# Kernel tuning notes

Hardware: AMD Instinct MI355X
Metric: run time of the kernel (lower is better)

## Reference

```python
import jax, jax.numpy as jnp
import numpy as np

C = 256
C8 = C // 8

def setup_inputs() -> dict:
    key = jax.random.key(0)
    ks = jax.random.split(key, 8)
    a = jax.random.normal(ks[0], (4, C, 64, 64), dtype=jnp.float32)
    s = 1.0 / np.sqrt(C)
    b_w = jax.random.normal(ks[1], (C8, C), dtype=jnp.float32) * s
    b_b = jnp.zeros((C8,), dtype=jnp.float32)
    c_w = jax.random.normal(ks[2], (C8, C), dtype=jnp.float32) * s
    c_b = jnp.zeros((C8,), dtype=jnp.float32)
    d_w = jax.random.normal(ks[3], (C, C), dtype=jnp.float32) * s
    d_b = jnp.zeros((C,), dtype=jnp.float32)
    alpha = jnp.zeros((1,), dtype=jnp.float32) + 0.5  # nonzero so attention path is exercised
    return {"a": a, "b_w": b_w, "b_b": b_b, "c_w": c_w, "c_b": c_b, "d_w": d_w, "d_b": d_b, "alpha": alpha}

def _conv1x1(x, w, b):
    # x: [n, c, h, w], w: [o, c] -> [n, o, h, w]
    return jnp.einsum('nchw,oc->nohw', x, w) + b[None, :, None, None]

def reference(a, b_w, b_b, c_w, c_b, d_w, d_b, alpha):
    n, chan, h, w = a.shape
    nhw = h * w
    b = _conv1x1(a, b_w, b_b).reshape(n, -1, nhw)   # [n, C/8, nhw]
    c = _conv1x1(a, c_w, c_b).reshape(n, -1, nhw)   # [n, C/8, nhw]
    k = jnp.einsum('nci,ncj->nij', b, c)            # [n, nhw, nhw]
    s = jax.nn.softmax(k, axis=-1)
    d = _conv1x1(a, d_w, d_b).reshape(n, -1, nhw)   # [n, C, nhw]
    kl = jnp.einsum('ncj,nij->nci', d, s)           # d @ s^T
    kl = kl.reshape(n, chan, h, w)
    return alpha * kl + a
```

## Files before the change

### kernel.cpp

```cpp
#include <hip/hip_runtime.h>
#include <hip/hip_bf16.h>

#define CCH 256
#define CQK 32
#define NHW 4096

typedef float f32x4 __attribute__((ext_vector_type(4)));
typedef _Float16 hv8 __attribute__((ext_vector_type(8)));
typedef _Float16 hv4 __attribute__((ext_vector_type(4)));
typedef __fp16 fv2 __attribute__((ext_vector_type(2)));

typedef __attribute__((address_space(3))) unsigned int lds_u32_t;
typedef __attribute__((address_space(1))) const unsigned int glb_u32_t;
__device__ __forceinline__ void gll16(const _Float16* gp, _Float16* lp) {
    __builtin_amdgcn_global_load_lds((glb_u32_t*)gp, (lds_u32_t*)lp, 16, 0, 0);
}

__global__ __launch_bounds__(256) void prep_kernel(
    const float* __restrict__ b_w, const float* __restrict__ c_w,
    const float* __restrict__ d_w, _Float16* __restrict__ Wh)
{
    const int bid = blockIdx.x, tid = threadIdx.x;
    const int idx = (bid * 256 + tid) * 4;
    const int row = idx >> 8, col = idx & 255;
    const float* src = (row < 32) ? (b_w + row * CCH + col)
                     : (row < 64) ? (c_w + (row - 32) * CCH + col)
                                  : (d_w + (row - 64) * CCH + col);
    const float scl = (row < 32) ? 1.4426950408889634f : 1.0f;
    float4 v = *reinterpret_cast<const float4*>(src);
    _Float16* dst = Wh + (size_t)row * CCH + col;
    dst[0] = (_Float16)(v.x * scl); dst[1] = (_Float16)(v.y * scl);
    dst[2] = (_Float16)(v.z * scl); dst[3] = (_Float16)(v.w * scl);
}

__global__ __launch_bounds__(256) void proj_kernel(
    const float* __restrict__ a, const _Float16* __restrict__ Wh,
    const float* __restrict__ b_b, const float* __restrict__ c_b,
    const float* __restrict__ d_b,
    _Float16* __restrict__ bqT, _Float16* __restrict__ ckT,
    _Float16* __restrict__ dv)
{
    __shared__ _Float16 aT[32][CCH + 24];

    const int n    = blockIdx.x >> 7;
    const int i0   = (blockIdx.x & 127) << 5;
    const int tid  = threadIdx.x;
    const int lane = tid & 63;
    const int wave = tid >> 6;
    const int l15  = lane & 15;
    const int quad = lane >> 4;

    {
        const float* ap = a + (size_t)(n*CCH + tid)*NHW + i0;
        #pragma unroll
        for (int j = 0; j < 8; ++j) {
            float4 v = *reinterpret_cast<const float4*>(ap + j*4);
            aT[j*4+0][tid] = (_Float16)v.x;
            aT[j*4+1][tid] = (_Float16)v.y;
            aT[j*4+2][tid] = (_Float16)v.z;
            aT[j*4+3][tid] = (_Float16)v.w;
        }
    }
    __syncthreads();

    const f32x4 zf = {0.f, 0.f, 0.f, 0.f};
    f32x4 acc[5][2];
    #pragma unroll
    for (int t = 0; t < 5; ++t) { acc[t][0] = zf; acc[t][1] = zf; }

    const int ch0w = wave * 80;

    #pragma unroll
    for (int ks = 0; ks < 8; ++ks) {
        const int k0 = ks * 32;
        hv8 af0 = *reinterpret_cast<const hv8*>(&aT[l15][k0 + quad*8]);
        hv8 af1 = *reinterpret_cast<const hv8*>(&aT[16 + l15][k0 + quad*8]);
        #pragma unroll
        for (int t = 0; t < 5; ++t) {
            const int ch0 = ch0w + t*16;
            hv8 bf = *reinterpret_cast<const hv8*>(
                Wh + (size_t)(ch0 + l15)*CCH + k0 + quad*8);
            acc[t][0] = __builtin_amdgcn_mfma_f32_16x16x32_f16(af0, bf, acc[t][0], 0, 0, 0);
            acc[t][1] = __builtin_amdgcn_mfma_f32_16x16x32_f16(af1, bf, acc[t][1], 0, 0, 0);
        }
    }

    const int pos_b = i0 + quad*4;
    #pragma unroll
    for (int t = 0; t < 5; ++t) {
        const int ch0 = ch0w + t*16;
        if (ch0 < 64) {
            const float* bias_arr = (ch0 < 32) ? b_b : c_b;
            _Float16*    outp     = (ch0 < 32) ? bqT : ckT;
            const int    ch       = (ch0 & 31) + l15;
            const float  bias     = bias_arr[ch] *
                ((ch0 < 32) ? 1.4426950408889634f : 1.0f);
            #pragma unroll
            for (int nf = 0; nf < 2; ++nf) {
                #pragma unroll
                for (int r = 0; r < 4; ++r) {
                    const int pos = pos_b + nf*16 + r;
                    outp[((size_t)n*NHW + pos)*CQK + ch] =
                        (_Float16)(acc[t][nf][r] + bias);
                }
            }
        } else {
            const int ch   = ch0 - 64 + l15;
            const float bias = d_b[ch];
            #pragma unroll
            for (int nf = 0; nf < 2; ++nf) {
                hv4 v = { (_Float16)(acc[t][nf][0] + bias),
                          (_Float16)(acc[t][nf][1] + bias),
                          (_Float16)(acc[t][nf][2] + bias),
                          (_Float16)(acc[t][nf][3] + bias) };
                *reinterpret_cast<hv4*>(
                    dv + ((size_t)n*CCH + ch)*NHW + pos_b + nf*16) = v;
            }
        }
    }
}

__global__ __launch_bounds__(512, 2) void attn_kernel(
    const _Float16* __restrict__ bqT, const _Float16* __restrict__ ckT,
    const _Float16* __restrict__ dv,
    const float* __restrict__ a, const float* __restrict__ alpha_p,
    float* __restrict__ out)
{
    __shared__ __align__(16) char smem[143360];

    const int bx   = ((blockIdx.x & 7) << 5) | (blockIdx.x >> 3);
    const int n    = bx >> 6;
    const int cg   = (bx >> 5) & 1;
    const int qt   = bx & 31;
    const int q0b  = qt << 7;
    const int co0  = cg << 7;
    const int tid  = threadIdx.x;
    const int wave = tid >> 6;
    const int g    = wave >> 1;
    const int qw   = wave & 1;
    const int lane = tid & 63;
    const int l15  = lane & 15;
    const int quad = lane >> 4;
    const int kg0  = g << 10;

    _Float16* vbuf = (_Float16*)(smem + (g << 14));
    _Float16* pb   = (_Float16*)(smem + 65536 + wave*9216);
    float*    lbuf = (float*)(smem + 139264);
    float*    mbuf = (float*)(smem + 141312);

    const f32x4 zf = {0.f, 0.f, 0.f, 0.f};
    const _Float16 one_h = (_Float16)1.0f;
    const hv8 ones = { one_h, one_h, one_h, one_h, one_h, one_h, one_h, one_h };

    hv8 qf[4];
    #pragma unroll
    for (int X = 0; X < 4; ++X) {
        const int q = q0b + qw*64 + X*16 + l15;
        qf[X] = *reinterpret_cast<const hv8*>(
            bqT + ((size_t)n*NHW + q)*CQK + quad*8);
    }

    const _Float16* ckbase = ckT + ((size_t)(n*NHW + kg0 + l15))*CQK + quad*8;

    float mneg[4] = {0.f, 0.f, 0.f, 0.f};

    f32x4 acc[4][8];
    #pragma unroll
    for (int X = 0; X < 4; ++X)
        #pragma unroll
        for (int t = 0; t < 8; ++t) acc[X][t] = zf;
    f32x4 accL[4];
    #pragma unroll
    for (int X = 0; X < 4; ++X) accL[X] = zf;

    const int rl8 = lane >> 3;
    const _Float16* dvs = dv
        + (size_t)(n*CCH + co0 + qw*64 + rl8)*NHW + kg0 + 8*((lane & 7) ^ rl8);
    _Float16* ldsb = (_Float16*)(smem + (g << 14) + qw*8192);

    const int c0h = ((quad*16) ^ ((l15 & 7) << 4)) >> 1;
    const int c1h = ((64 + quad*16) ^ ((l15 & 7) << 4)) >> 1;

    auto softmax_tile = [&](const hv8* kf) {
        #pragma unroll
        for (int X = 0; X < 4; ++X) {
            const f32x4 minit = {mneg[X], mneg[X], mneg[X], mneg[X]};
            f32x4 s0 = __builtin_amdgcn_mfma_f32_16x16x32_f16(kf[0], qf[X], minit, 0, 0, 0);
            f32x4 s1 = __builtin_amdgcn_mfma_f32_16x16x32_f16(kf[1], qf[X], minit, 0, 0, 0);
            f32x4 s2 = __builtin_amdgcn_mfma_f32_16x16x32_f16(kf[2], qf[X], minit, 0, 0, 0);
            f32x4 s3 = __builtin_amdgcn_mfma_f32_16x16x32_f16(kf[3], qf[X], minit, 0, 0, 0);
            float tm = fmaxf(
                fmaxf(fmaxf(fmaxf(s0[0], s0[1]), fmaxf(s0[2], s0[3])),
                      fmaxf(fmaxf(s1[0], s1[1]), fmaxf(s1[2], s1[3]))),
                fmaxf(fmaxf(fmaxf(s2[0], s2[1]), fmaxf(s2[2], s2[3])),
                      fmaxf(fmaxf(s3[0], s3[1]), fmaxf(s3[2], s3[3]))));
            tm = fmaxf(tm, __shfl_xor(tm, 16, 64));
            tm = fmaxf(tm, __shfl_xor(tm, 32, 64));
            const float upd = (tm > 8.0f) ? tm : 0.0f;
            if (__any(upd > 0.0f)) {
                const float sc = __builtin_amdgcn_exp2f(-upd);
                float s_r0 = __shfl(sc, quad*4 + 0, 64);
                float s_r1 = __shfl(sc, quad*4 + 1, 64);
                float s_r2 = __shfl(sc, quad*4 + 2, 64);
                float s_r3 = __shfl(sc, quad*4 + 3, 64);
                #pragma unroll
                for (int t = 0; t < 8; ++t) {
                    acc[X][t][0] *= s_r0; acc[X][t][1] *= s_r1;
                    acc[X][t][2] *= s_r2; acc[X][t][3] *= s_r3;
                }
                accL[X][0] *= s_r0; accL[X][1] *= s_r1;
                accL[X][2] *= s_r2; accL[X][3] *= s_r3;
                mneg[X] -= upd;
                s0[0] -= upd; s0[1] -= upd; s0[2] -= upd; s0[3] -= upd;
                s1[0] -= upd; s1[1] -= upd; s1[2] -= upd; s1[3] -= upd;
                s2[0] -= upd; s2[1] -= upd; s2[2] -= upd; s2[3] -= upd;
                s3[0] -= upd; s3[1] -= upd; s3[2] -= upd; s3[3] -= upd;
            }
            const f32x4 sv[4] = {s0, s1, s2, s3};
            #pragma unroll
            for (int f = 0; f < 4; ++f) {
                float p0 = __builtin_amdgcn_exp2f(sv[f][0]);
                float p1 = __builtin_amdgcn_exp2f(sv[f][1]);
                float p2 = __builtin_amdgcn_exp2f(sv[f][2]);
                float p3 = __builtin_amdgcn_exp2f(sv[f][3]);
                fv2 lo = __builtin_amdgcn_cvt_pkrtz(p0, p1);
                fv2 hi = __builtin_amdgcn_cvt_pkrtz(p2, p3);
                uint2 w;
                w.x = __builtin_bit_cast(unsigned, lo);
                w.y = __builtin_bit_cast(unsigned, hi);
                *reinterpret_cast<uint2*>(
                    pb + X*1152 + l15*72 + f*16 + quad*4) = w;
            }
        }
    };

    hv8 pf0[4], pf1[4];
    auto read_pf = [&]() {
        #pragma unroll
        for (int X = 0; X < 4; ++X) {
            pf0[X] = *reinterpret_cast<const hv8*>(pb + X*1152 + l15*72 + quad*8);
            pf1[X] = *reinterpret_cast<const hv8*>(pb + X*1152 + l15*72 + 32 + quad*8);
        }
    };

    auto stage = [&](int kt) {
        #pragma unroll
        for (int j = 0; j < 8; ++j)
            gll16(dvs + (size_t)(j*8)*NHW + kt*64, ldsb + (size_t)(j*8)*64);
    };

    auto load_kf = [&](int key0, hv8* kf) {
        #pragma unroll
        for (int f = 0; f < 4; ++f)
            kf[f] = *reinterpret_cast<const hv8*>(
                ckbase + (size_t)(key0 + f*16)*CQK);
    };

    {
        stage(0);
        hv8 kf0[4];
        load_kf(0, kf0);
        softmax_tile(kf0);
        read_pf();
    }
    __syncthreads();

    for (int kt = 0; kt < 16; ++kt) {
        hv8 kfn[4];
        if (kt < 15) load_kf((kt + 1)*64, kfn);

        #pragma unroll
        for (int t = 0; t < 8; ++t) {
            const _Float16* vr = vbuf + (t*16 + l15)*64;
            hv8 d0 = *reinterpret_cast<const hv8*>(vr + c0h);
            #pragma unroll
            for (int X = 0; X < 4; ++X)
                acc[X][t] = __builtin_amdgcn_mfma_f32_16x16x32_f16(
                    pf0[X], d0, acc[X][t], 0, 0, 0);
            hv8 d1 = *reinterpret_cast<const hv8*>(vr + c1h);
            #pragma unroll
            for (int X = 0; X < 4; ++X)
                acc[X][t] = __builtin_amdgcn_mfma_f32_16x16x32_f16(
                    pf1[X], d1, acc[X][t], 0, 0, 0);
        }
        #pragma unroll
        for (int X = 0; X < 4; ++X) {
            accL[X] = __builtin_amdgcn_mfma_f32_16x16x32_f16(pf0[X], ones, accL[X], 0, 0, 0);
            accL[X] = __builtin_amdgcn_mfma_f32_16x16x32_f16(pf1[X], ones, accL[X], 0, 0, 0);
        }

        if (kt < 15) {
            softmax_tile(kfn);
            __syncthreads();
            stage(kt + 1);
            read_pf();
            __syncthreads();
        }
    }

    if (lane < 16) {
        #pragma unroll
        for (int X = 0; X < 4; ++X)
            mbuf[g*128 + qw*64 + X*16 + l15] = -mneg[X];
    }
    __syncthreads();

    {
        #pragma unroll
        for (int X = 0; X < 4; ++X) {
            const int qloc = qw*64 + X*16 + quad*4;
            float4 m0 = *reinterpret_cast<float4*>(&mbuf[0*128 + qloc]);
            float4 m1 = *reinterpret_cast<float4*>(&mbuf[1*128 + qloc]);
            float4 m2 = *reinterpret_cast<float4*>(&mbuf[2*128 + qloc]);
            float4 m3 = *reinterpret_cast<float4*>(&mbuf[3*128 + qloc]);
            float4 mm;
            mm.x = fmaxf(fmaxf(m0.x, m1.x), fmaxf(m2.x, m3.x));
            mm.y = fmaxf(fmaxf(m0.y, m1.y), fmaxf(m2.y, m3.y));
            mm.z = fmaxf(fmaxf(m0.z, m1.z), fmaxf(m2.z, m3.z));
            mm.w = fmaxf(fmaxf(m0.w, m1.w), fmaxf(m2.w, m3.w));
            float4 mo = (g == 0) ? m0 : (g == 1) ? m1 : (g == 2) ? m2 : m3;
            float sc0 = __builtin_amdgcn_exp2f(mo.x - mm.x);
            float sc1 = __builtin_amdgcn_exp2f(mo.y - mm.y);
            float sc2 = __builtin_amdgcn_exp2f(mo.z - mm.z);
            float sc3 = __builtin_amdgcn_exp2f(mo.w - mm.w);
            #pragma unroll
            for (int t = 0; t < 8; ++t) {
                acc[X][t][0] *= sc0; acc[X][t][1] *= sc1;
                acc[X][t][2] *= sc2; acc[X][t][3] *= sc3;
            }
            accL[X][0] *= sc0; accL[X][1] *= sc1;
            accL[X][2] *= sc2; accL[X][3] *= sc3;
        }
    }

    float* buf1 = (float*)smem;
    float* buf2 = (float*)(smem + 67584);
    const int qloc = qw*64 + quad*4;

    if (l15 == 0) {
        #pragma unroll
        for (int X = 0; X < 4; ++X)
            *reinterpret_cast<float4*>(&lbuf[g*128 + qw*64 + X*16 + quad*4]) =
                *reinterpret_cast<float4*>(&accL[X]);
    }
    if (g == 1 || g == 3) {
        float* b = (g == 1) ? buf1 : buf2;
        #pragma unroll
        for (int X = 0; X < 4; ++X)
            #pragma unroll
            for (int t = 0; t < 8; ++t)
                *reinterpret_cast<float4*>(
                    &b[(t*16 + l15)*132 + qw*64 + X*16 + quad*4]) =
                    *reinterpret_cast<float4*>(&acc[X][t]);
    }
    __syncthreads();
    if (g == 0 || g == 2) {
        float* b = (g == 0) ? buf1 : buf2;
        #pragma unroll
        for (int X = 0; X < 4; ++X)
            #pragma unroll
            for (int t = 0; t < 8; ++t) {
                float4 p = *reinterpret_cast<float4*>(
                    &b[(t*16 + l15)*132 + qw*64 + X*16 + quad*4]);
                acc[X][t][0] += p.x; acc[X][t][1] += p.y;
                acc[X][t][2] += p.z; acc[X][t][3] += p.w;
            }
    }
    __syncthreads();
    if (g == 2) {
        #pragma unroll
        for (int X = 0; X < 4; ++X)
            #pragma unroll
            for (int t = 0; t < 8; ++t)
                *reinterpret_cast<float4*>(
                    &buf1[(t*16 + l15)*132 + qw*64 + X*16 + quad*4]) =
                    *reinterpret_cast<float4*>(&acc[X][t]);
    }
    __syncthreads();
    if (g == 0) {
        const float alpha = alpha_p[0];
        #pragma unroll
        for (int X = 0; X < 4; ++X) {
            const int qlocX = qw*64 + X*16 + quad*4;
            #pragma unroll
            for (int t = 0; t < 8; ++t) {
                float4 p = *reinterpret_cast<float4*>(
                    &buf1[(t*16 + l15)*132 + qlocX]);
                acc[X][t][0] += p.x; acc[X][t][1] += p.y;
                acc[X][t][2] += p.z; acc[X][t][3] += p.w;
            }
            float4 l0 = *reinterpret_cast<float4*>(&lbuf[0*128 + qlocX]);
            float4 l1 = *reinterpret_cast<float4*>(&lbuf[1*128 + qlocX]);
            float4 l2 = *reinterpret_cast<float4*>(&lbuf[2*128 + qlocX]);
            float4 l3 = *reinterpret_cast<float4*>(&lbuf[3*128 + qlocX]);
            f32x4 rl;
            rl[0] = alpha / (l0.x + l1.x + l2.x + l3.x);
            rl[1] = alpha / (l0.y + l1.y + l2.y + l3.y);
            rl[2] = alpha / (l0.z + l1.z + l2.z + l3.z);
            rl[3] = alpha / (l0.w + l1.w + l2.w + l3.w);
            #pragma unroll
            for (int t = 0; t < 8; ++t) {
                const size_t off =
                    ((size_t)(n*CCH + co0 + t*16 + l15))*NHW + q0b + qlocX;
                float4 av = *reinterpret_cast<const float4*>(a + off);
                float4 o;
                o.x = acc[X][t][0]*rl[0] + av.x;
                o.y = acc[X][t][1]*rl[1] + av.y;
                o.z = acc[X][t][2]*rl[2] + av.z;
                o.w = acc[X][t][3]*rl[3] + av.w;
                *reinterpret_cast<float4*>(out + off) = o;
            }
        }
    }
}

extern "C" void kernel_launch(void* const* d_in, const int* in_sizes, int n_in,
                              void* d_out, int out_size, void* d_ws, size_t ws_size,
                              hipStream_t stream)
{
    const float* a    = (const float*)d_in[0];
    const float* b_w  = (const float*)d_in[1];
    const float* b_b  = (const float*)d_in[2];
    const float* c_w  = (const float*)d_in[3];
    const float* c_b  = (const float*)d_in[4];
    const float* d_w  = (const float*)d_in[5];
    const float* d_b  = (const float*)d_in[6];
    const float* alp  = (const float*)d_in[7];
    float* out = (float*)d_out;

    _Float16* bqT  = (_Float16*)d_ws;
    _Float16* ckT  = bqT + (size_t)4*NHW*CQK;
    _Float16* dv   = ckT + (size_t)4*NHW*CQK;
    _Float16* Wh   = dv + (size_t)4*CCH*NHW;

    prep_kernel<<<80, 256, 0, stream>>>(b_w, c_w, d_w, Wh);
    proj_kernel<<<512, 256, 0, stream>>>(a, Wh, b_b, c_b, d_b, bqT, ckT, dv);
    attn_kernel<<<256, 512, 0, stream>>>(bqT, ckT, dv, a, alp, out);
}
```

Before: 165.0 us.

## Halve key tile to 32 and double-buffer V staging with one barrier per step

The key tile per iteration shrinks from 64 to 32 keys, so each step runs half the QK and PV MFMAs. The V tile staging becomes double-buffered: the next tile's global-to-LDS load is issued at the top of the iteration and overlaps the current compute. This removes one of the two __syncthreads per step, and the per-wave P buffer shrinks. The trade-off is twice as many iterations, more frequent softmax max checks and barriers, and shorter runs of MFMA work per sync.

After: 174.5 us. +5.8%, slower.

```diff
diff --git a/kernel.cpp b/kernel.cpp
--- a/kernel.cpp
+++ b/kernel.cpp
@@ -143,8 +143,7 @@
     const int quad = lane >> 4;
     const int kg0  = g << 10;
 
-    _Float16* vbuf = (_Float16*)(smem + (g << 14));
-    _Float16* pb   = (_Float16*)(smem + 65536 + wave*9216);
+    _Float16* pb   = (_Float16*)(smem + 65536 + wave*5120);
     float*    lbuf = (float*)(smem + 139264);
     float*    mbuf = (float*)(smem + 141312);
 
@@ -173,13 +172,12 @@
     #pragma unroll
     for (int X = 0; X < 4; ++X) accL[X] = zf;
 
-    const int rl8 = lane >> 3;
+    const int rl4 = lane >> 2;
+    const int sl  = lane & 3;
     const _Float16* dvs = dv
-        + (size_t)(n*CCH + co0 + qw*64 + rl8)*NHW + kg0 + 8*((lane & 7) ^ rl8);
-    _Float16* ldsb = (_Float16*)(smem + (g << 14) + qw*8192);
-
-    const int c0h = ((quad*16) ^ ((l15 & 7) << 4)) >> 1;
-    const int c1h = ((64 + quad*16) ^ ((l15 & 7) << 4)) >> 1;
+        + (size_t)(n*CCH + co0 + qw*64 + rl4)*NHW + kg0 + 8*(sl ^ ((rl4 >> 1) & 3));
+
+    const int c0h = (quad*8) ^ (((l15 >> 1) & 3) << 3);
 
     auto softmax_tile = [&](const hv8* kf) {
         #pragma unroll
@@ -187,13 +185,9 @@
             const f32x4 minit = {mneg[X], mneg[X], mneg[X], mneg[X]};
             f32x4 s0 = __builtin_amdgcn_mfma_f32_16x16x32_f16(kf[0], qf[X], minit, 0, 0, 0);
             f32x4 s1 = __builtin_amdgcn_mfma_f32_16x16x32_f16(kf[1], qf[X], minit, 0, 0, 0);
-            f32x4 s2 = __builtin_amdgcn_mfma_f32_16x16x32_f16(kf[2], qf[X], minit, 0, 0, 0);
-            f32x4 s3 = __builtin_amdgcn_mfma_f32_16x16x32_f16(kf[3], qf[X], minit, 0, 0, 0);
             float tm = fmaxf(
-                fmaxf(fmaxf(fmaxf(s0[0], s0[1]), fmaxf(s0[2], s0[3])),
-                      fmaxf(fmaxf(s1[0], s1[1]), fmaxf(s1[2], s1[3]))),
-                fmaxf(fmaxf(fmaxf(s2[0], s2[1]), fmaxf(s2[2], s2[3])),
-                      fmaxf(fmaxf(s3[0], s3[1]), fmaxf(s3[2], s3[3]))));
+                fmaxf(fmaxf(s0[0], s0[1]), fmaxf(s0[2], s0[3])),
+                fmaxf(fmaxf(s1[0], s1[1]), fmaxf(s1[2], s1[3])));
             tm = fmaxf(tm, __shfl_xor(tm, 16, 64));
             tm = fmaxf(tm, __shfl_xor(tm, 32, 64));
             const float upd = (tm > 8.0f) ? tm : 0.0f;
@@ -213,12 +207,10 @@
                 mneg[X] -= upd;
                 s0[0] -= upd; s0[1] -= upd; s0[2] -= upd; s0[3] -= upd;
                 s1[0] -= upd; s1[1] -= upd; s1[2] -= upd; s1[3] -= upd;
-                s2[0] -= upd; s2[1] -= upd; s2[2] -= upd; s2[3] -= upd;
-                s3[0] -= upd; s3[1] -= upd; s3[2] -= upd; s3[3] -= upd;
-            }
-            const f32x4 sv[4] = {s0, s1, s2, s3};
-            #pragma unroll
-            for (int f = 0; f < 4; ++f) {
+            }
+            const f32x4 sv[2] = {s0, s1};
+            #pragma unroll
+            for (int f = 0; f < 2; ++f) {
                 float p0 = __builtin_amdgcn_exp2f(sv[f][0]);
                 float p1 = __builtin_amdgcn_exp2f(sv[f][1]);
                 float p2 = __builtin_amdgcn_exp2f(sv[f][2]);
@@ -229,73 +221,68 @@
                 w.x = __builtin_bit_cast(unsigned, lo);
                 w.y = __builtin_bit_cast(unsigned, hi);
                 *reinterpret_cast<uint2*>(
-                    pb + X*1152 + l15*72 + f*16 + quad*4) = w;
+                    pb + X*640 + l15*40 + f*16 + quad*4) = w;
             }
         }
     };
 
-    hv8 pf0[4], pf1[4];
+    hv8 pf0[4];
     auto read_pf = [&]() {
         #pragma unroll
-        for (int X = 0; X < 4; ++X) {
-            pf0[X] = *reinterpret_cast<const hv8*>(pb + X*1152 + l15*72 + quad*8);
-            pf1[X] = *reinterpret_cast<const hv8*>(pb + X*1152 + l15*72 + 32 + quad*8);
-        }
+        for (int X = 0; X < 4; ++X)
+            pf0[X] = *reinterpret_cast<const hv8*>(pb + X*640 + l15*40 + quad*8);
     };
 
-    auto stage = [&](int kt) {
-        #pragma unroll
-        for (int j = 0; j < 8; ++j)
-            gll16(dvs + (size_t)(j*8)*NHW + kt*64, ldsb + (size_t)(j*8)*64);
+    auto stage = [&](int kt, int b) {
+        _Float16* ldsb = (_Float16*)(smem + (g*2 + b)*8192) + qw*2048;
+        #pragma unroll
+        for (int j = 0; j < 4; ++j)
+            gll16(dvs + (size_t)(j*16)*NHW + kt*32, ldsb + j*512);
     };
 
     auto load_kf = [&](int key0, hv8* kf) {
         #pragma unroll
-        for (int f = 0; f < 4; ++f)
+        for (int f = 0; f < 2; ++f)
             kf[f] = *reinterpret_cast<const hv8*>(
                 ckbase + (size_t)(key0 + f*16)*CQK);
     };
 
     {
-        stage(0);
-        hv8 kf0[4];
+        stage(0, 0);
+        hv8 kf0[2];
         load_kf(0, kf0);
         softmax_tile(kf0);
         read_pf();
     }
     __syncthreads();
 
-    for (int kt = 0; kt < 16; ++kt) {
-        hv8 kfn[4];
-        if (kt < 15) load_kf((kt + 1)*64, kfn);
-
+    int cur = 0;
+    for (int kt = 0; kt < 32; ++kt) {
+        hv8 kfn[2];
+        if (kt < 31) {
+            stage(kt + 1, cur ^ 1);
+            load_kf((kt + 1)*32, kfn);
+        }
+
+        const _Float16* vb = (const _Float16*)(smem + (g*2 + cur)*8192);
         #pragma unroll
         for (int t = 0; t < 8; ++t) {
-            const _Float16* vr = vbuf + (t*16 + l15)*64;
-            hv8 d0 = *reinterpret_cast<const hv8*>(vr + c0h);
+            hv8 d0 = *reinterpret_cast<const hv8*>(vb + (t*16 + l15)*32 + c0h);
             #pragma unroll
             for (int X = 0; X < 4; ++X)
                 acc[X][t] = __builtin_amdgcn_mfma_f32_16x16x32_f16(
                     pf0[X], d0, acc[X][t], 0, 0, 0);
-            hv8 d1 = *reinterpret_cast<const hv8*>(vr + c1h);
-            #pragma unroll
-            for (int X = 0; X < 4; ++X)
-                acc[X][t] = __builtin_amdgcn_mfma_f32_16x16x32_f16(
-                    pf1[X], d1, acc[X][t], 0, 0, 0);
-        }
-        #pragma unroll
-        for (int X = 0; X < 4; ++X) {
+        }
+        #pragma unroll
+        for (int X = 0; X < 4; ++X)
             accL[X] = __builtin_amdgcn_mfma_f32_16x16x32_f16(pf0[X], ones, accL[X], 0, 0, 0);
-            accL[X] = __builtin_amdgcn_mfma_f32_16x16x32_f16(pf1[X], ones, accL[X], 0, 0, 0);
-        }
-
-        if (kt < 15) {
+
+        if (kt < 31) {
             softmax_tile(kfn);
-            __syncthreads();
-            stage(kt + 1);
             read_pf();
             __syncthreads();
         }
+        cur ^= 1;
     }
 
     if (lane < 16) {
@@ -335,7 +322,6 @@
 
     float* buf1 = (float*)smem;
     float* buf2 = (float*)(smem + 67584);
-    const int qloc = qw*64 + quad*4;
 
     if (l15 == 0) {
         #pragma unroll
```
